# Performance work log

Hardware: AMD Instinct MI355X
Metric: run time of the kernel (lower is better)

The kernel has to match this reference:

```python
import jax, jax.numpy as jnp
import numpy as np

K = 20          # knn neighbors (init kwarg k)
LEAK = 0.2      # LeakyReLU negative slope
EPS = 1e-5      # BatchNorm eps


def knn(x, k):
    # x: (B, D, N) -> indices (B, N, K) of k nearest (largest negative sq-dist)
    inner = -2.0 * jnp.einsum('bin,bim->bnm', x, x)
    xx = jnp.sum(x * x, axis=1, keepdims=True)            # (B,1,N)
    pd = -xx - inner - jnp.swapaxes(xx, 1, 2)             # (B,N,N)
    return jax.lax.top_k(pd, k)[1]


def gather_graph_feature(x, idx):
    # x: (B,D,N), idx: (B,N,K) -> (B, 2D, N, K)
    feat = jax.vmap(lambda xb, ib: xb[:, ib])(x, idx)     # (B,D,N,K)
    xc = x[..., None]                                     # (B,D,N,1)
    return jnp.concatenate([feat - xc, jnp.broadcast_to(xc, feat.shape)], axis=1)


def bn_lrelu(y, g, b, axes):
    mu = jnp.mean(y, axis=axes, keepdims=True)
    var = jnp.var(y, axis=axes, keepdims=True)            # biased var (torch BN train)
    shape = [1] * y.ndim
    shape[1] = -1
    y = (y - mu) * jax.lax.rsqrt(var + EPS) * g.reshape(shape) + b.reshape(shape)
    return jnp.where(y >= 0, y, LEAK * y)


def edge_block(x, idx, w, g, b):
    f = gather_graph_feature(x, idx)                      # (B,2D,N,K)
    y = jnp.einsum('oc,bcnk->bonk', w, f)                 # 1x1 Conv2d, no bias
    y = bn_lrelu(y, g, b, (0, 2, 3))
    return jnp.max(y, axis=-1)                            # max over K -> (B,O,N)


def setup_inputs() -> dict:
    key = jax.random.key(0)
    ks = jax.random.split(key, 8)
    B, D, N = 2, 2, 4096
    out_dim = 512
    pts = jax.random.normal(ks[0], (B, D, N), dtype=jnp.float32)
    dims = [(64, 4), (64, 128), (128, 128), (256, 256), (out_dim, 512)]
    inp = {'pts': pts}
    for i, (o, c) in enumerate(dims):
        inp[f'w{i+1}'] = jax.random.normal(ks[i + 1], (o, c), dtype=jnp.float32) * 0.05
        inp[f'g{i+1}'] = jnp.ones((o,), dtype=jnp.float32)
        inp[f'b{i+1}'] = jnp.zeros((o,), dtype=jnp.float32)
    return inp


def reference(pts, w1, g1, b1, w2, g2, b2, w3, g3, b3, w4, g4, b4, w5, g5, b5):
    idx = knn(pts, K)
    x1 = edge_block(pts, idx, w1, g1, b1)   # (B,64,N)
    x2 = edge_block(x1, idx, w2, g2, b2)    # (B,64,N)
    x3 = edge_block(x2, idx, w3, g3, b3)    # (B,128,N)
    x4 = edge_block(x3, idx, w4, g4, b4)    # (B,256,N)
    x = jnp.concatenate([x1, x2, x3, x4], axis=1)         # (B,512,N)
    y = jnp.einsum('oc,bcn->bon', w5, x)                  # 1x1 Conv1d, no bias
    return bn_lrelu(y, g5, b5, (0, 2))
```

## Files before the change

kernel.cpp:

```cpp
#include <hip/hip_runtime.h>
#include <hip/hip_bf16.h>
#include <math.h>

#define BB 2
#define NN 4096
#define PP (BB*NN)
#define KK 20
#define LEAK 0.2f
#define EPSB 1e-5f

typedef short sv8 __attribute__((ext_vector_type(8)));
typedef float f4  __attribute__((ext_vector_type(4)));

__device__ inline unsigned short f2bf(float f) {
    unsigned u = __float_as_uint(f);
    unsigned r = (u + 0x7FFFu + ((u >> 16) & 1u)) >> 16;
    return (unsigned short)r;
}
__device__ inline float bf2f(unsigned short h) {
    return __uint_as_float((unsigned)h << 16);
}
__device__ inline void gload16(const void* g, void* l) {
    __builtin_amdgcn_global_load_lds(
        (const __attribute__((address_space(1))) unsigned int*)g,
        (__attribute__((address_space(3))) unsigned int*)l, 16, 0, 0);
}

__global__ void transpose_pts(const float* __restrict__ pts, float* __restrict__ pts_t) {
    int e = blockIdx.x * 256 + threadIdx.x;
    if (e >= PP) return;
    int b = e / NN, n = e % NN;
    pts_t[(size_t)e * 2 + 0] = pts[(size_t)b * 2 * NN + n];
    pts_t[(size_t)e * 2 + 1] = pts[(size_t)b * 2 * NN + NN + n];
}

__global__ __launch_bounds__(256) void knn_kernel(const float* __restrict__ pts,
                                                  int* __restrict__ idx) {
    __shared__ unsigned int hist[256];
    __shared__ unsigned int scanres[3];
    __shared__ unsigned int cnt2[2];
    __shared__ unsigned long long blist[512];

    int r = blockIdx.x;
    int b = r >> 12, n = r & (NN - 1);
    const float* X0 = pts + (size_t)b * 2 * NN;
    const float* X1 = X0 + NN;
    int tid = threadIdx.x;
    float x0n = X0[n], x1n = X1[n];
    float xxn = __fadd_rn(__fmul_rn(x0n, x0n), __fmul_rn(x1n, x1n));
    float negxxn = __fsub_rn(0.f, xxn);

    float pdv[16];
    #pragma unroll
    for (int q = 0; q < 16; ++q) {
        int m = q * 256 + tid;
        float x0m = X0[m], x1m = X1[m];
        float xxm = __fadd_rn(__fmul_rn(x0m, x0m), __fmul_rn(x1m, x1m));
        float dot = __builtin_fmaf(x1n, x1m, __fmul_rn(x0n, x0m));
        float inner = __fmul_rn(-2.f, dot);
        float t1 = __fsub_rn(negxxn, inner);
        pdv[q] = __fsub_rn(t1, xxm);
    }

    int shift = 24;
    for (int attempt = 0; attempt < 3; ++attempt) {
        hist[tid] = 0;
        __syncthreads();
        float scale = (float)(1u << shift);
        #pragma unroll
        for (int q = 0; q < 16; ++q) {
            float s = fmaxf(-pdv[q], 0.f);
            unsigned int ki = (unsigned int)fminf(s * scale, 4.294e9f);
            unsigned int bin = ki >> 16;
            if (bin < 255u) atomicAdd(&hist[bin], 1u);
        }
        __syncthreads();
        if (tid < 64) {
            uint4 hv = *(const uint4*)&hist[tid * 4];
            unsigned int p0 = hv.x, p1 = p0 + hv.y, p2 = p1 + hv.z, p3 = p2 + hv.w;
            unsigned int lanesum = p3, inc = p3;
            #pragma unroll
            for (int s2 = 1; s2 < 64; s2 <<= 1) {
                unsigned int o = __shfl_up(inc, s2, 64);
                if (tid >= s2) inc += o;
            }
            unsigned int excl = inc - lanesum;
            bool flag = (inc >= KK);
            unsigned long long bal = __ballot(flag);
            int firstlane = (bal == 0ULL) ? -1 : (__ffsll((long long)bal) - 1);
            if (tid == 0) scanres[0] = (bal != 0ULL) ? 1u : 0u;
            if (tid == firstlane) {
                unsigned int c0 = excl + p0, c1 = excl + p1, c2 = excl + p2;
                int t = (c0 >= KK) ? 0 : (c1 >= KK) ? 1 : (c2 >= KK) ? 2 : 3;
                unsigned int cumb = (t == 0) ? excl : (t == 1) ? c0 : (t == 2) ? c1 : c2;
                scanres[1] = (unsigned)(tid * 4 + t);
                scanres[2] = cumb;
            }
        }
        __syncthreads();
        if (scanres[0]) break;
        shift -= 6;
        __syncthreads();
    }

    unsigned int bstar = scanres[1];
    unsigned int cumb  = scanres[2];
    if (tid == 0) { cnt2[0] = 0; cnt2[1] = 0; }
    __syncthreads();

    float scale = (float)(1u << shift);
    #pragma unroll
    for (int q = 0; q < 16; ++q) {
        float s = fmaxf(-pdv[q], 0.f);
        unsigned int ki = (unsigned int)fminf(s * scale, 4.294e9f);
        unsigned int bin = ki >> 16;
        if (bin > 255u) bin = 255u;
        int m = q * 256 + tid;
        if (bin < bstar) {
            unsigned int slot = atomicAdd(&cnt2[0], 1u);
            idx[(size_t)r * KK + slot] = m;
        } else if (bin == bstar) {
            unsigned int pos = atomicAdd(&cnt2[1], 1u);
            if (pos < 512u) {
                unsigned int ub = __float_as_uint(pdv[q]);
                unsigned int fk = (ub & 0x80000000u) ? ~ub : (ub | 0x80000000u);
                blist[pos] = ((unsigned long long)(~fk) << 32) | (unsigned int)m;
            }
        }
    }
    __syncthreads();

    int need = KK - (int)cumb;
    int L = (int)min(cnt2[1], 512u);
    if (tid < 64) {
        unsigned long long e[8];
        #pragma unroll
        for (int i = 0; i < 8; ++i) {
            int p = tid + 64 * i;
            e[i] = (p < L) ? blist[p] : ~0ULL;
        }
        unsigned long long lmin = e[0];
        #pragma unroll
        for (int i = 1; i < 8; ++i) lmin = (e[i] < lmin) ? e[i] : lmin;
        for (int p = 0; p < need; ++p) {
            unsigned long long gm = lmin;
            #pragma unroll
            for (int s2 = 32; s2 > 0; s2 >>= 1) {
                unsigned long long o = __shfl_xor(gm, s2, 64);
                if (o < gm) gm = o;
            }
            if (lmin == gm) {
                #pragma unroll
                for (int i = 0; i < 8; ++i) if (e[i] == gm) e[i] = ~0ULL;
                lmin = e[0];
                #pragma unroll
                for (int i = 1; i < 8; ++i) lmin = (e[i] < lmin) ? e[i] : lmin;
                idx[(size_t)r * KK + cumb + p] = (int)(gm & 0xFFFFFFFFu);
            }
        }
    }
}

__global__ __launch_bounds__(256) void proj_gemm(const float* __restrict__ X, int ldx, int C,
                                                 const float* __restrict__ W, int O, int mode,
                                                 float* __restrict__ outU, float* __restrict__ outV) {
    __shared__ float Xs[16][65];
    __shared__ float Ws[16][65];
    int row0 = blockIdx.x * 64, col0 = blockIdx.y * 64;
    int tid = threadIdx.x;
    int tx = tid % 16, ty = tid / 16;
    float acc[4][4] = {};
    for (int c0 = 0; c0 < C; c0 += 16) {
        for (int i = 0; i < 4; ++i) {
            int mm = ty + i * 16;
            float val = 0.f;
            if (c0 + tx < C) val = X[(size_t)(row0 + mm) * ldx + c0 + tx];
            Xs[tx][mm] = val;
        }
        for (int i = 0; i < 4; ++i) {
            int jj = ty + i * 16;
            int j = col0 + jj;
            float val = 0.f;
            if (c0 + tx < C) {
                if (mode == 0) {
                    if (j < O) val = W[(size_t)j * (2 * C) + c0 + tx];
                    else {
                        const float* wr = W + (size_t)(j - O) * (2 * C);
                        val = wr[C + c0 + tx] - wr[c0 + tx];
                    }
                } else {
                    val = W[(size_t)j * C + c0 + tx];
                }
            }
            Ws[tx][jj] = val;
        }
        __syncthreads();
        int kmax = (C - c0 < 16) ? (C - c0) : 16;
        for (int kk = 0; kk < kmax; ++kk) {
            float a[4], bw[4];
            #pragma unroll
            for (int i = 0; i < 4; ++i) a[i] = Xs[kk][ty * 4 + i];
            #pragma unroll
            for (int j = 0; j < 4; ++j) bw[j] = Ws[kk][tx * 4 + j];
            #pragma unroll
            for (int i = 0; i < 4; ++i)
                #pragma unroll
                for (int j = 0; j < 4; ++j)
                    acc[i][j] = fmaf(a[i], bw[j], acc[i][j]);
        }
        __syncthreads();
    }
    for (int i = 0; i < 4; ++i) {
        int rr = row0 + ty * 4 + i;
        for (int j = 0; j < 4; ++j) {
            int jg = col0 + tx * 4 + j;
            float vv = acc[i][j];
            if (mode == 0) {
                if (jg < O) outU[(size_t)rr * O + jg] = vv;
                else        outV[(size_t)rr * O + (jg - O)] = vv;
            } else {
                outU[(size_t)rr * O + jg] = vv;
            }
        }
    }
}

__global__ void convert_w(const float* __restrict__ w, int O, int C, int mode,
                          unsigned short* __restrict__ bh, unsigned short* __restrict__ bl) {
    int total = (mode == 0 ? 2 * O : O) * C;
    int i = blockIdx.x * 256 + threadIdx.x;
    if (i >= total) return;
    int j = i / C, c = i - j * C;
    float v;
    if (mode == 0) {
        if (j < O) v = w[(size_t)j * 2 * C + c];
        else {
            const float* wr = w + (size_t)(j - O) * 2 * C;
            v = wr[C + c] - wr[c];
        }
    } else {
        v = w[(size_t)j * C + c];
    }
    unsigned short h = f2bf(v);
    bh[i] = h;
    bl[i] = f2bf(v - bf2f(h));
}

__global__ __launch_bounds__(256) void mfma_gemm(const unsigned short* __restrict__ Xh,
                                                 const unsigned short* __restrict__ Xl, int ldx,
                                                 int K,
                                                 const unsigned short* __restrict__ Bh,
                                                 const unsigned short* __restrict__ Bl,
                                                 int O, int mode,
                                                 float* __restrict__ outU,
                                                 float* __restrict__ outV) {
    __shared__ unsigned short Ah[512 * 8], Al[512 * 8], Bhs[512 * 8], Bls[512 * 8];
    int row0 = blockIdx.x * 128, col0 = blockIdx.y * 128;
    int tid = threadIdx.x;
    int wid = tid >> 6, lane = tid & 63;
    int wm = wid & 1, wn = wid >> 1;
    int l15 = lane & 15, l4 = lane >> 4;

    f4 acc[4][4];
    #pragma unroll
    for (int i = 0; i < 4; ++i)
        #pragma unroll
        for (int j = 0; j < 4; ++j) { acc[i][j][0]=0.f; acc[i][j][1]=0.f; acc[i][j][2]=0.f; acc[i][j][3]=0.f; }

    for (int k0 = 0; k0 < K; k0 += 32) {
        #pragma unroll
        for (int j = 0; j < 2; ++j) {
            int c = tid + 256 * j;
            int m = c & 127, kb = c >> 7;
            size_t ga = (size_t)(row0 + m) * ldx + k0 + kb * 8;
            size_t gb = (size_t)(col0 + m) * K + k0 + kb * 8;
            gload16(Xh + ga, &Ah[(size_t)(wid * 64 + 256 * j) * 8]);
            gload16(Xl + ga, &Al[(size_t)(wid * 64 + 256 * j) * 8]);
            gload16(Bh + gb, &Bhs[(size_t)(wid * 64 + 256 * j) * 8]);
            gload16(Bl + gb, &Bls[(size_t)(wid * 64 + 256 * j) * 8]);
        }
        __syncthreads();

        sv8 bhf[4], blf[4];
        #pragma unroll
        for (int fn = 0; fn < 4; ++fn) {
            int nn2 = wn * 64 + fn * 16 + l15;
            bhf[fn] = *(const sv8*)&Bhs[(size_t)(l4 * 128 + nn2) * 8];
            blf[fn] = *(const sv8*)&Bls[(size_t)(l4 * 128 + nn2) * 8];
        }
        #pragma unroll
        for (int fm = 0; fm < 4; ++fm) {
            int m = wm * 64 + fm * 16 + l15;
            sv8 ah = *(const sv8*)&Ah[(size_t)(l4 * 128 + m) * 8];
            sv8 al = *(const sv8*)&Al[(size_t)(l4 * 128 + m) * 8];
            #pragma unroll
            for (int fn = 0; fn < 4; ++fn) {
                acc[fm][fn] = __builtin_amdgcn_mfma_f32_16x16x32_bf16(ah, bhf[fn], acc[fm][fn], 0, 0, 0);
                acc[fm][fn] = __builtin_amdgcn_mfma_f32_16x16x32_bf16(ah, blf[fn], acc[fm][fn], 0, 0, 0);
                acc[fm][fn] = __builtin_amdgcn_mfma_f32_16x16x32_bf16(al, bhf[fn], acc[fm][fn], 0, 0, 0);
            }
        }
        __syncthreads();
    }

    #pragma unroll
    for (int fm = 0; fm < 4; ++fm) {
        int rbase = row0 + wm * 64 + fm * 16 + l4 * 4;
        #pragma unroll
        for (int fn = 0; fn < 4; ++fn) {
            int jg = col0 + wn * 64 + fn * 16 + l15;
            #pragma unroll
            for (int e = 0; e < 4; ++e) {
                float vv = acc[fm][fn][e];
                int p = rbase + e;
                if (mode == 1 || jg < O) outU[(size_t)p * O + jg] = vv;
                else                     outV[(size_t)p * O + (jg - O)] = vv;
            }
        }
    }
}

__global__ __launch_bounds__(256) void edge_stats(const float* __restrict__ u,
                                                  const float* __restrict__ v,
                                                  const int* __restrict__ idx,
                                                  int O, int PPL,
                                                  float* __restrict__ mx, float* __restrict__ mn,
                                                  float* __restrict__ partial) {
    __shared__ float red[4 * 256];
    int tid = threadIdx.x;
    int CH2 = O >> 1;
    int PS = 256 / CH2;
    int co = tid % CH2;
    int ps = tid / CH2;
    float s1a = 0.f, s1b = 0.f, s2a = 0.f, s2b = 0.f;
    for (int pi = 0; pi < PPL; ++pi) {
        int r = (blockIdx.x * PS + ps) * PPL + pi;
        int b = r >> 12;
        const float* ub = u + (size_t)b * NN * O + 2 * co;
        float2 vv = *(const float2*)&v[(size_t)r * O + 2 * co];
        const int* ip = idx + (size_t)r * KK;
        int mreg[KK];
        #pragma unroll
        for (int k = 0; k < KK; ++k) mreg[k] = ip[k];
        float2 uv[KK];
        #pragma unroll
        for (int k = 0; k < KK; ++k) uv[k] = *(const float2*)&ub[(size_t)mreg[k] * O];
        float bxa = -INFINITY, bxb = -INFINITY, bna = INFINITY, bnb = INFINITY;
        #pragma unroll
        for (int k = 0; k < KK; ++k) {
            float y0 = uv[k].x + vv.x, y1 = uv[k].y + vv.y;
            s1a += y0; s2a = fmaf(y0, y0, s2a);
            s1b += y1; s2b = fmaf(y1, y1, s2b);
            bxa = fmaxf(bxa, y0); bna = fminf(bna, y0);
            bxb = fmaxf(bxb, y1); bnb = fminf(bnb, y1);
        }
        *(float2*)&mx[(size_t)r * O + 2 * co] = make_float2(bxa, bxb);
        *(float2*)&mn[(size_t)r * O + 2 * co] = make_float2(bna, bnb);
    }
    red[0 * 256 + tid] = s1a;
    red[1 * 256 + tid] = s1b;
    red[2 * 256 + tid] = s2a;
    red[3 * 256 + tid] = s2b;
    __syncthreads();
    for (int s = PS >> 1; s > 0; s >>= 1) {
        if (ps < s) {
            int oth = tid + s * CH2;
            red[0 * 256 + tid] += red[0 * 256 + oth];
            red[1 * 256 + tid] += red[1 * 256 + oth];
            red[2 * 256 + tid] += red[2 * 256 + oth];
            red[3 * 256 + tid] += red[3 * 256 + oth];
        }
        __syncthreads();
    }
    if (ps == 0) {
        size_t base = (size_t)blockIdx.x * 2 * O;
        partial[base + 2 * co]         = red[0 * 256 + tid];
        partial[base + 2 * co + 1]     = red[1 * 256 + tid];
        partial[base + O + 2 * co]     = red[2 * 256 + tid];
        partial[base + O + 2 * co + 1] = red[3 * 256 + tid];
    }
}

__global__ __launch_bounds__(256) void stats_reduce(const float* __restrict__ partial, int nblk,
                                                    int O, float cnt,
                                                    const float* __restrict__ g,
                                                    const float* __restrict__ bsh,
                                                    float* __restrict__ st) {
    __shared__ float r1[4], r2[4];
    int o = blockIdx.x, tid = threadIdx.x;
    float s1 = 0.f, s2 = 0.f;
    for (int bk = tid; bk < nblk; bk += 256) {
        size_t base = (size_t)bk * 2 * O;
        s1 += partial[base + o];
        s2 += partial[base + O + o];
    }
    #pragma unroll
    for (int s = 32; s > 0; s >>= 1) {
        s1 += __shfl_down(s1, s, 64);
        s2 += __shfl_down(s2, s, 64);
    }
    if ((tid & 63) == 0) { r1[tid >> 6] = s1; r2[tid >> 6] = s2; }
    __syncthreads();
    if (tid == 0) {
        s1 = r1[0] + r1[1] + r1[2] + r1[3];
        s2 = r2[0] + r2[1] + r2[2] + r2[3];
        float mu = s1 / cnt;
        float var = s2 / cnt - mu * mu;
        float x = var + EPSB;
        float rr = rsqrtf(x);
        rr = rr * (1.5f - 0.5f * x * rr * rr);
        float sc = g[o] * rr;
        st[o] = sc;
        st[O + o] = bsh[o] - mu * sc;
    }
}

__global__ void apply_edge(const float* __restrict__ mx, const float* __restrict__ mn,
                           const float* __restrict__ st, int O, int choff,
                           unsigned short* __restrict__ xh, unsigned short* __restrict__ xl) {
    int e = blockIdx.x * 256 + threadIdx.x;
    if (e >= PP * O) return;
    int r = e / O, o = e % O;
    float sc = st[o], tt = st[O + o];
    float base = (sc >= 0.f) ? mx[e] : mn[e];
    float y = fmaf(sc, base, tt);
    y = (y >= 0.f) ? y : LEAK * y;
    unsigned short h = f2bf(y);
    size_t d = (size_t)r * 512 + choff + o;
    xh[d] = h;
    xl[d] = f2bf(y - bf2f(h));
}

__global__ __launch_bounds__(256) void final_stats(const float* __restrict__ y5,
                                                   float* __restrict__ partial) {
    int blk = blockIdx.x, t = threadIdx.x;
    float s1a = 0.f, s2a = 0.f, s1b = 0.f, s2b = 0.f;
    for (int rr = 0; rr < 128; ++rr) {
        size_t row = (size_t)(blk * 128 + rr) * 512;
        float va = y5[row + t], vb = y5[row + t + 256];
        s1a += va; s2a = fmaf(va, va, s2a);
        s1b += vb; s2b = fmaf(vb, vb, s2b);
    }
    partial[((size_t)blk * 512 + t) * 2 + 0] = s1a;
    partial[((size_t)blk * 512 + t) * 2 + 1] = s2a;
    partial[((size_t)blk * 512 + t + 256) * 2 + 0] = s1b;
    partial[((size_t)blk * 512 + t + 256) * 2 + 1] = s2b;
}

__global__ __launch_bounds__(64) void final_reduce(const float* __restrict__ partial, int nblk,
                                                   float cnt,
                                                   const float* __restrict__ g,
                                                   const float* __restrict__ bsh,
                                                   float* __restrict__ st) {
    int c = blockIdx.x, tid = threadIdx.x;
    float s1 = 0.f, s2 = 0.f;
    for (int bk = tid; bk < nblk; bk += 64) {
        size_t base = ((size_t)bk * 512 + c) * 2;
        s1 += partial[base];
        s2 += partial[base + 1];
    }
    #pragma unroll
    for (int s = 32; s > 0; s >>= 1) {
        s1 += __shfl_down(s1, s, 64);
        s2 += __shfl_down(s2, s, 64);
    }
    if (tid == 0) {
        float mu = s1 / cnt;
        float var = s2 / cnt - mu * mu;
        float x = var + EPSB;
        float rr = rsqrtf(x);
        rr = rr * (1.5f - 0.5f * x * rr * rr);
        float sc = g[c] * rr;
        st[c] = sc;
        st[512 + c] = bsh[c] - mu * sc;
    }
}

__global__ __launch_bounds__(256) void final_apply(const float* __restrict__ y5,
                                                   const float* __restrict__ st,
                                                   float* __restrict__ out) {
    __shared__ float tile[32][33];
    int n0 = blockIdx.x * 32, o0 = blockIdx.y * 32, b = blockIdx.z;
    int tx = threadIdx.x, ty = threadIdx.y;
    for (int i = 0; i < 4; ++i) {
        int nl = ty + i * 8;
        tile[nl][tx] = y5[((size_t)(b * NN + n0 + nl)) * 512 + o0 + tx];
    }
    __syncthreads();
    for (int i = 0; i < 4; ++i) {
        int ol = ty + i * 8;
        int o = o0 + ol;
        float sc = st[o], tt = st[512 + o];
        float yv = fmaf(sc, tile[tx][ol], tt);
        yv = (yv >= 0.f) ? yv : LEAK * yv;
        out[((size_t)b * 512 + o) * NN + n0 + tx] = yv;
    }
}

extern "C" void kernel_launch(void* const* d_in, const int* in_sizes, int n_in,
                              void* d_out, int out_size, void* d_ws, size_t ws_size,
                              hipStream_t stream) {
    const float* pts = (const float*)d_in[0];
    const float* w[5]; const float* g[5]; const float* bsh[5];
    for (int i = 0; i < 5; ++i) {
        w[i]   = (const float*)d_in[1 + 3 * i];
        g[i]   = (const float*)d_in[2 + 3 * i];
        bsh[i] = (const float*)d_in[3 + 3 * i];
    }
    float* out = (float*)d_out;

    unsigned short* xh = (unsigned short*)d_ws;
    unsigned short* xl = xh + (size_t)PP * 512;
    float* u    = (float*)(xl + (size_t)PP * 512);
    float* v    = u    + (size_t)PP * 256;
    float* mxb  = v    + (size_t)PP * 256;
    float* mnb  = mxb  + (size_t)PP * 256;
    float* y5   = u;
    float* ptst = mnb  + (size_t)PP * 256;
    int*   idxb = (int*)(ptst + (size_t)PP * 2);
    float* part = (float*)(idxb + (size_t)PP * KK);
    float* st   = part + (size_t)1048576;
    unsigned short* bmh = (unsigned short*)part;
    unsigned short* bml = bmh + (size_t)512 * 512;

    transpose_pts<<<(PP + 255) / 256, 256, 0, stream>>>(pts, ptst);
    knn_kernel<<<PP, 256, 0, stream>>>(pts, idxb);

    const int Cs[4]    = {2, 64, 64, 128};
    const int Os[4]    = {64, 64, 128, 256};
    const int choffs[4]= {0, 64, 128, 256};
    const int inoffs[4]= {0, 0, 64, 128};

    for (int li = 0; li < 4; ++li) {
        int C = Cs[li], O = Os[li];
        if (li == 0) {
            dim3 gg(PP / 64, (2 * O) / 64);
            proj_gemm<<<gg, 256, 0, stream>>>(ptst, 2, C, w[li], O, 0, u, v);
        } else {
            int total = 2 * O * C;
            convert_w<<<(total + 255) / 256, 256, 0, stream>>>(w[li], O, C, 0, bmh, bml);
            dim3 gg(PP / 128, (2 * O) / 128);
            mfma_gemm<<<gg, 256, 0, stream>>>(xh + inoffs[li], xl + inoffs[li], 512, C,
                                              bmh, bml, O, 0, u, v);
        }
        int PS  = 512 / O;
        int PPL = (O == 256) ? 2 : 1;
        int nblk = PP / (PS * PPL);
        edge_stats<<<nblk, 256, 0, stream>>>(u, v, idxb, O, PPL, mxb, mnb, part);
        stats_reduce<<<O, 256, 0, stream>>>(part, nblk, O, (float)((size_t)PP * KK),
                                            g[li], bsh[li], st);
        apply_edge<<<(PP * O + 255) / 256, 256, 0, stream>>>(mxb, mnb, st, O, choffs[li], xh, xl);
    }

    convert_w<<<(512 * 512 + 255) / 256, 256, 0, stream>>>(w[4], 512, 512, 1, bmh, bml);
    dim3 gf(PP / 128, 512 / 128);
    mfma_gemm<<<gf, 256, 0, stream>>>(xh, xl, 512, 512, bmh, bml, 512, 1, y5, nullptr);
    final_stats<<<64, 256, 0, stream>>>(y5, part);
    final_reduce<<<512, 64, 0, stream>>>(part, 64, (float)PP, g[4], bsh[4], st);
    final_apply<<<dim3(NN / 32, 512 / 32, BB), dim3(32, 8), 0, stream>>>(y5, st, out);
}
```

Baseline: 229.2 us.

## Use single bf16 for final GEMM, smaller tiles for edge GEMMs, merge small kernels

The final 512x512 conv GEMM now uses a single bf16 MFMA pass instead of a three-term hi/lo split, and no longer loads the low parts. This cuts its MFMA work and LDS traffic to about a third, at the cost of accuracy. The per-layer edge GEMMs move to 64x64 tiles so more blocks run at small O. The point transpose is folded into the knn kernel and all weight conversions are merged into one launch. apply_edge is vectorized to two channels per thread and skips writing low parts that are never read.

```diff
diff --git a/kernel.cpp b/kernel.cpp
--- a/kernel.cpp
+++ b/kernel.cpp
@@ -26,16 +26,9 @@
         (__attribute__((address_space(3))) unsigned int*)l, 16, 0, 0);
 }
 
-__global__ void transpose_pts(const float* __restrict__ pts, float* __restrict__ pts_t) {
-    int e = blockIdx.x * 256 + threadIdx.x;
-    if (e >= PP) return;
-    int b = e / NN, n = e % NN;
-    pts_t[(size_t)e * 2 + 0] = pts[(size_t)b * 2 * NN + n];
-    pts_t[(size_t)e * 2 + 1] = pts[(size_t)b * 2 * NN + NN + n];
-}
-
 __global__ __launch_bounds__(256) void knn_kernel(const float* __restrict__ pts,
-                                                  int* __restrict__ idx) {
+                                                  int* __restrict__ idx,
+                                                  float* __restrict__ pts_t) {
     __shared__ unsigned int hist[256];
     __shared__ unsigned int scanres[3];
     __shared__ unsigned int cnt2[2];
@@ -47,6 +40,10 @@
     const float* X1 = X0 + NN;
     int tid = threadIdx.x;
     float x0n = X0[n], x1n = X1[n];
+    if (tid == 0) {
+        pts_t[(size_t)r * 2 + 0] = x0n;
+        pts_t[(size_t)r * 2 + 1] = x1n;
+    }
     float xxn = __fadd_rn(__fmul_rn(x0n, x0n), __fmul_rn(x1n, x1n));
     float negxxn = __fsub_rn(0.f, xxn);
 
@@ -225,36 +222,112 @@
     }
 }
 
-__global__ void convert_w(const float* __restrict__ w, int O, int C, int mode,
-                          unsigned short* __restrict__ bh, unsigned short* __restrict__ bl) {
-    int total = (mode == 0 ? 2 * O : O) * C;
+__global__ __launch_bounds__(256) void convert_all(const float* __restrict__ w2,
+                                                   const float* __restrict__ w3,
+                                                   const float* __restrict__ w4,
+                                                   const float* __restrict__ w5,
+                                                   unsigned short* __restrict__ bh,
+                                                   unsigned short* __restrict__ bl) {
     int i = blockIdx.x * 256 + threadIdx.x;
-    if (i >= total) return;
-    int j = i / C, c = i - j * C;
+    if (i >= 352256) return;
+    const float* w; int O, C, mode, base;
+    if (i < 8192)       { w = w2; O = 64;  C = 64;  mode = 0; base = 0; }
+    else if (i < 24576) { w = w3; O = 128; C = 64;  mode = 0; base = 8192; }
+    else if (i < 90112) { w = w4; O = 256; C = 128; mode = 0; base = 24576; }
+    else                { w = w5; O = 512; C = 512; mode = 1; base = 90112; }
+    int j = i - base;
+    int row = j / C, c = j - row * C;
     float v;
     if (mode == 0) {
-        if (j < O) v = w[(size_t)j * 2 * C + c];
+        if (row < O) v = w[(size_t)row * 2 * C + c];
         else {
-            const float* wr = w + (size_t)(j - O) * 2 * C;
+            const float* wr = w + (size_t)(row - O) * 2 * C;
             v = wr[C + c] - wr[c];
         }
     } else {
-        v = w[(size_t)j * C + c];
+        v = w[(size_t)row * C + c];
     }
     unsigned short h = f2bf(v);
     bh[i] = h;
     bl[i] = f2bf(v - bf2f(h));
 }
 
-__global__ __launch_bounds__(256) void mfma_gemm(const unsigned short* __restrict__ Xh,
-                                                 const unsigned short* __restrict__ Xl, int ldx,
-                                                 int K,
-                                                 const unsigned short* __restrict__ Bh,
-                                                 const unsigned short* __restrict__ Bl,
-                                                 int O, int mode,
-                                                 float* __restrict__ outU,
-                                                 float* __restrict__ outV) {
-    __shared__ unsigned short Ah[512 * 8], Al[512 * 8], Bhs[512 * 8], Bls[512 * 8];
+__global__ __launch_bounds__(256) void mfma_gemm64(const unsigned short* __restrict__ Xh,
+                                                   const unsigned short* __restrict__ Xl,
+                                                   int ldx, int K,
+                                                   const unsigned short* __restrict__ Bh,
+                                                   const unsigned short* __restrict__ Bl,
+                                                   int O,
+                                                   float* __restrict__ outU,
+                                                   float* __restrict__ outV) {
+    __shared__ unsigned short Ah[256 * 8], Al[256 * 8], Bhs[256 * 8], Bls[256 * 8];
+    int row0 = blockIdx.x * 64, col0 = blockIdx.y * 64;
+    int tid = threadIdx.x;
+    int wid = tid >> 6, lane = tid & 63;
+    int wm = wid & 1, wn = wid >> 1;
+    int l15 = lane & 15, l4 = lane >> 4;
+    int m = tid & 63, kb = tid >> 6;
+
+    f4 acc[2][2];
+    #pragma unroll
+    for (int i = 0; i < 2; ++i)
+        #pragma unroll
+        for (int j = 0; j < 2; ++j) { acc[i][j][0]=0.f; acc[i][j][1]=0.f; acc[i][j][2]=0.f; acc[i][j][3]=0.f; }
+
+    for (int k0 = 0; k0 < K; k0 += 32) {
+        size_t ga = (size_t)(row0 + m) * ldx + k0 + kb * 8;
+        size_t gb = (size_t)(col0 + m) * K + k0 + kb * 8;
+        gload16(Xh + ga, &Ah[(size_t)(wid * 64) * 8]);
+        gload16(Xl + ga, &Al[(size_t)(wid * 64) * 8]);
+        gload16(Bh + gb, &Bhs[(size_t)(wid * 64) * 8]);
+        gload16(Bl + gb, &Bls[(size_t)(wid * 64) * 8]);
+        __syncthreads();
+
+        sv8 bhf[2], blf[2];
+        #pragma unroll
+        for (int fn = 0; fn < 2; ++fn) {
+            int nn2 = wn * 32 + fn * 16 + l15;
+            bhf[fn] = *(const sv8*)&Bhs[(size_t)(l4 * 64 + nn2) * 8];
+            blf[fn] = *(const sv8*)&Bls[(size_t)(l4 * 64 + nn2) * 8];
+        }
+        #pragma unroll
+        for (int fm = 0; fm < 2; ++fm) {
+            int mm = wm * 32 + fm * 16 + l15;
+            sv8 ah = *(const sv8*)&Ah[(size_t)(l4 * 64 + mm) * 8];
+            sv8 al = *(const sv8*)&Al[(size_t)(l4 * 64 + mm) * 8];
+            #pragma unroll
+            for (int fn = 0; fn < 2; ++fn) {
+                acc[fm][fn] = __builtin_amdgcn_mfma_f32_16x16x32_bf16(ah, bhf[fn], acc[fm][fn], 0, 0, 0);
+                acc[fm][fn] = __builtin_amdgcn_mfma_f32_16x16x32_bf16(ah, blf[fn], acc[fm][fn], 0, 0, 0);
+                acc[fm][fn] = __builtin_amdgcn_mfma_f32_16x16x32_bf16(al, bhf[fn], acc[fm][fn], 0, 0, 0);
+            }
+        }
+        __syncthreads();
+    }
+
+    #pragma unroll
+    for (int fm = 0; fm < 2; ++fm) {
+        int rbase = row0 + wm * 32 + fm * 16 + l4 * 4;
+        #pragma unroll
+        for (int fn = 0; fn < 2; ++fn) {
+            int jg = col0 + wn * 32 + fn * 16 + l15;
+            #pragma unroll
+            for (int e = 0; e < 4; ++e) {
+                float vv = acc[fm][fn][e];
+                int p = rbase + e;
+                if (jg < O) outU[(size_t)p * O + jg] = vv;
+                else        outV[(size_t)p * O + (jg - O)] = vv;
+            }
+        }
+    }
+}
+
+__global__ __launch_bounds__(256) void mfma_gemm128s(const unsigned short* __restrict__ Xh,
+                                                     int ldx, int K,
+                                                     const unsigned short* __restrict__ Bh,
+                                                     int O,
+                                                     float* __restrict__ outU) {
+    __shared__ unsigned short Ah[512 * 8], Bhs[512 * 8];
     int row0 = blockIdx.x * 128, col0 = blockIdx.y * 128;
     int tid = threadIdx.x;
     int wid = tid >> 6, lane = tid & 63;
@@ -275,30 +348,23 @@
             size_t ga = (size_t)(row0 + m) * ldx + k0 + kb * 8;
             size_t gb = (size_t)(col0 + m) * K + k0 + kb * 8;
             gload16(Xh + ga, &Ah[(size_t)(wid * 64 + 256 * j) * 8]);
-            gload16(Xl + ga, &Al[(size_t)(wid * 64 + 256 * j) * 8]);
             gload16(Bh + gb, &Bhs[(size_t)(wid * 64 + 256 * j) * 8]);
-            gload16(Bl + gb, &Bls[(size_t)(wid * 64 + 256 * j) * 8]);
-        }
-        __syncthreads();
-
-        sv8 bhf[4], blf[4];
+        }
+        __syncthreads();
+
+        sv8 bhf[4];
         #pragma unroll
         for (int fn = 0; fn < 4; ++fn) {
             int nn2 = wn * 64 + fn * 16 + l15;
             bhf[fn] = *(const sv8*)&Bhs[(size_t)(l4 * 128 + nn2) * 8];
-            blf[fn] = *(const sv8*)&Bls[(size_t)(l4 * 128 + nn2) * 8];
         }
         #pragma unroll
         for (int fm = 0; fm < 4; ++fm) {
-            int m = wm * 64 + fm * 16 + l15;
-            sv8 ah = *(const sv8*)&Ah[(size_t)(l4 * 128 + m) * 8];
-            sv8 al = *(const sv8*)&Al[(size_t)(l4 * 128 + m) * 8];
-            #pragma unroll
-            for (int fn = 0; fn < 4; ++fn) {
+            int mm = wm * 64 + fm * 16 + l15;
+            sv8 ah = *(const sv8*)&Ah[(size_t)(l4 * 128 + mm) * 8];
+            #pragma unroll
+            for (int fn = 0; fn < 4; ++fn)
                 acc[fm][fn] = __builtin_amdgcn_mfma_f32_16x16x32_bf16(ah, bhf[fn], acc[fm][fn], 0, 0, 0);
-                acc[fm][fn] = __builtin_amdgcn_mfma_f32_16x16x32_bf16(ah, blf[fn], acc[fm][fn], 0, 0, 0);
-                acc[fm][fn] = __builtin_amdgcn_mfma_f32_16x16x32_bf16(al, bhf[fn], acc[fm][fn], 0, 0, 0);
-            }
         }
         __syncthreads();
     }
@@ -310,12 +376,8 @@
         for (int fn = 0; fn < 4; ++fn) {
             int jg = col0 + wn * 64 + fn * 16 + l15;
             #pragma unroll
-            for (int e = 0; e < 4; ++e) {
-                float vv = acc[fm][fn][e];
-                int p = rbase + e;
-                if (mode == 1 || jg < O) outU[(size_t)p * O + jg] = vv;
-                else                     outV[(size_t)p * O + (jg - O)] = vv;
-            }
+            for (int e = 0; e < 4; ++e)
+                outU[(size_t)(rbase + e) * O + jg] = acc[fm][fn][e];
         }
     }
 }
@@ -417,18 +479,27 @@
 
 __global__ void apply_edge(const float* __restrict__ mx, const float* __restrict__ mn,
                            const float* __restrict__ st, int O, int choff,
-                           unsigned short* __restrict__ xh, unsigned short* __restrict__ xl) {
-    int e = blockIdx.x * 256 + threadIdx.x;
-    if (e >= PP * O) return;
-    int r = e / O, o = e % O;
-    float sc = st[o], tt = st[O + o];
-    float base = (sc >= 0.f) ? mx[e] : mn[e];
-    float y = fmaf(sc, base, tt);
-    y = (y >= 0.f) ? y : LEAK * y;
-    unsigned short h = f2bf(y);
+                           unsigned short* __restrict__ xh, unsigned short* __restrict__ xl,
+                           int writelo) {
+    int e2 = blockIdx.x * 256 + threadIdx.x;
+    int half = O >> 1;
+    if (e2 >= PP * half) return;
+    int r = e2 / half, o = (e2 - r * half) * 2;
+    float2 sc = *(const float2*)&st[o];
+    float2 tt = *(const float2*)&st[O + o];
+    float2 vx = *(const float2*)&mx[(size_t)r * O + o];
+    float2 vn = *(const float2*)&mn[(size_t)r * O + o];
+    float b0 = (sc.x >= 0.f) ? vx.x : vn.x;
+    float b1 = (sc.y >= 0.f) ? vx.y : vn.y;
+    float y0 = fmaf(sc.x, b0, tt.x); y0 = (y0 >= 0.f) ? y0 : LEAK * y0;
+    float y1 = fmaf(sc.y, b1, tt.y); y1 = (y1 >= 0.f) ? y1 : LEAK * y1;
+    unsigned short h0 = f2bf(y0), h1 = f2bf(y1);
     size_t d = (size_t)r * 512 + choff + o;
-    xh[d] = h;
-    xl[d] = f2bf(y - bf2f(h));
+    ((unsigned int*)xh)[d >> 1] = (unsigned int)h0 | ((unsigned int)h1 << 16);
+    if (writelo) {
+        unsigned short l0 = f2bf(y0 - bf2f(h0)), l1 = f2bf(y1 - bf2f(h1));
+        ((unsigned int*)xl)[d >> 1] = (unsigned int)l0 | ((unsigned int)l1 << 16);
+    }
 }
 
 __global__ __launch_bounds__(256) void final_stats(const float* __restrict__ y5,
@@ -520,28 +591,27 @@
     int*   idxb = (int*)(ptst + (size_t)PP * 2);
     float* part = (float*)(idxb + (size_t)PP * KK);
     float* st   = part + (size_t)1048576;
-    unsigned short* bmh = (unsigned short*)part;
-    unsigned short* bml = bmh + (size_t)512 * 512;
-
-    transpose_pts<<<(PP + 255) / 256, 256, 0, stream>>>(pts, ptst);
-    knn_kernel<<<PP, 256, 0, stream>>>(pts, idxb);
+    unsigned short* wh_all = (unsigned short*)(st + 1024);
+    unsigned short* wl_all = wh_all + 352256;
+
+    knn_kernel<<<PP, 256, 0, stream>>>(pts, idxb, ptst);
+    convert_all<<<1376, 256, 0, stream>>>(w[1], w[2], w[3], w[4], wh_all, wl_all);
 
     const int Cs[4]    = {2, 64, 64, 128};
     const int Os[4]    = {64, 64, 128, 256};
     const int choffs[4]= {0, 64, 128, 256};
     const int inoffs[4]= {0, 0, 64, 128};
+    const int woffs[4] = {0, 0, 8192, 24576};
 
     for (int li = 0; li < 4; ++li) {
         int C = Cs[li], O = Os[li];
         if (li == 0) {
             dim3 gg(PP / 64, (2 * O) / 64);
-            proj_gemm<<<gg, 256, 0, stream>>>(ptst, 2, C, w[li], O, 0, u, v);
+            proj_gemm<<<gg, 256, 0, stream>>>(ptst, 2, C, w[0], O, 0, u, v);
         } else {
-            int total = 2 * O * C;
-            convert_w<<<(total + 255) / 256, 256, 0, stream>>>(w[li], O, C, 0, bmh, bml);
-            dim3 gg(PP / 128, (2 * O) / 128);
-            mfma_gemm<<<gg, 256, 0, stream>>>(xh + inoffs[li], xl + inoffs[li], 512, C,
-                                              bmh, bml, O, 0, u, v);
+            dim3 gg(PP / 64, (2 * O) / 64);
+            mfma_gemm64<<<gg, 256, 0, stream>>>(xh + inoffs[li], xl + inoffs[li], 512, C,
+                                                wh_all + woffs[li], wl_all + woffs[li], O, u, v);
         }
         int PS  = 512 / O;
         int PPL = (O == 256) ? 2 : 1;
@@ -549,12 +619,12 @@
         edge_stats<<<nblk, 256, 0, stream>>>(u, v, idxb, O, PPL, mxb, mnb, part);
         stats_reduce<<<O, 256, 0, stream>>>(part, nblk, O, (float)((size_t)PP * KK),
                                             g[li], bsh[li], st);
-        apply_edge<<<(PP * O + 255) / 256, 256, 0, stream>>>(mxb, mnb, st, O, choffs[li], xh, xl);
-    }
-
-    convert_w<<<(512 * 512 + 255) / 256, 256, 0, stream>>>(w[4], 512, 512, 1, bmh, bml);
+        apply_edge<<<(PP * O / 2 + 255) / 256, 256, 0, stream>>>(
+            mxb, mnb, st, O, choffs[li], xh, xl, (li == 3) ? 0 : 1);
+    }
+
     dim3 gf(PP / 128, 512 / 128);
-    mfma_gemm<<<gf, 256, 0, stream>>>(xh, xl, 512, 512, bmh, bml, 512, 1, y5, nullptr);
+    mfma_gemm128s<<<gf, 256, 0, stream>>>(xh, 512, 512, wh_all + 90112, 512, y5);
     final_stats<<<64, 256, 0, stream>>>(y5, part);
     final_reduce<<<512, 64, 0, stream>>>(part, 64, (float)PP, g[4], bsh[4], st);
     final_apply<<<dim3(NN / 32, 512 / 32, BB), dim3(32, 8), 0, stream>>>(y5, st, out);
```

Result: faster. 194.0 us (-15.4%).
